# Kernel optimization log

Hardware: AMD Instinct MI355X
Metric: run time of the kernel (lower is better)

Reference implementation:

```python
import jax, jax.numpy as jnp
import numpy as np

BITS = 8
EPS = 1e-5
NUM_HEADS = 16


def ste_round(x):
    # straight-through rounding (matches brevitas round STE)
    return x + jax.lax.stop_gradient(jnp.round(x) - x)


def _scale(stat, qmax):
    return jnp.maximum(stat, 1e-8) / qmax


def fq_act_signed(x, bits=BITS):
    # runtime max-abs per-tensor scale (approximates brevitas runtime percentile 99.999)
    qmax = 2 ** (bits - 1) - 1
    qmin = -(2 ** (bits - 1))
    s = _scale(jnp.max(jnp.abs(x)), qmax)
    return jnp.clip(ste_round(x / s), qmin, qmax) * s


def fq_act_unsigned(x, bits=BITS):
    qmax = 2 ** bits - 1
    s = _scale(jnp.max(x), qmax)
    return jnp.clip(ste_round(x / s), 0, qmax) * s


def fq_weight(w, bits=BITS):
    # NarrowIntQuant + MaxStatsScaling: symmetric narrow range [-qmax, qmax]
    qmax = 2 ** (bits - 1) - 1
    s = _scale(jnp.max(jnp.abs(w)), qmax)
    return jnp.clip(ste_round(w / s), -qmax, qmax) * s


def fq_bias(b, bits=BITS):
    qmax = 2 ** (bits - 1) - 1
    qmin = -(2 ** (bits - 1))
    s = _scale(jnp.max(jnp.abs(b)), qmax)
    return jnp.clip(ste_round(b / s), qmin, qmax) * s


def layernorm(x):
    # elementwise_affine=False
    m = jnp.mean(x, axis=-1, keepdims=True)
    v = jnp.mean((x - m) ** 2, axis=-1, keepdims=True)
    return (x - m) / jnp.sqrt(v + EPS)


def setup_inputs() -> dict:
    key = jax.random.key(0)
    ks = jax.random.split(key, 13)
    B, S, E, M = 4, 1024, 1024, 4096
    std = 0.02
    inp = {
        "x": jax.random.normal(ks[0], (B, S, E), jnp.float32),
        "Wq": jax.random.normal(ks[1], (E, E), jnp.float32) * std,
        "bq": jax.random.normal(ks[2], (E,), jnp.float32) * std,
        "Wk": jax.random.normal(ks[3], (E, E), jnp.float32) * std,
        "bk": jax.random.normal(ks[4], (E,), jnp.float32) * std,
        "Wv": jax.random.normal(ks[5], (E, E), jnp.float32) * std,
        "bv": jax.random.normal(ks[6], (E,), jnp.float32) * std,
        "Wo": jax.random.normal(ks[7], (E, E), jnp.float32) * std,
        "bo": jax.random.normal(ks[8], (E,), jnp.float32) * std,
        "W1": jax.random.normal(ks[9], (M, E), jnp.float32) * std,
        "b1": jax.random.normal(ks[10], (M,), jnp.float32) * std,
        "W2": jax.random.normal(ks[11], (E, M), jnp.float32) * std,
        "b2": jax.random.normal(ks[12], (E,), jnp.float32) * std,
    }
    return inp


def reference(x, Wq, bq, Wk, bk, Wv, bv, Wo, bo, W1, b1, W2, b2):
    B, S, E = x.shape
    H = NUM_HEADS
    D = E // H
    # causal additive mask [S, S]
    i = jnp.arange(S)
    mask = jnp.where(i[None, :] <= i[:, None], 0.0, -jnp.inf).astype(x.dtype)

    # sdp_input_quant (shared q=k=v input)
    q_in = fq_act_signed(x)

    # quantized in-proj (packed_in_proj=False -> separate q/k/v projections)
    Q = q_in @ fq_weight(Wq).T + fq_bias(bq)
    K = q_in @ fq_weight(Wk).T + fq_bias(bk)
    V = q_in @ fq_weight(Wv).T + fq_bias(bv)

    Qh = Q.reshape(B, S, H, D)
    Kh = K.reshape(B, S, H, D)
    Vh = V.reshape(B, S, H, D)

    qs = fq_act_signed(Qh / jnp.sqrt(jnp.asarray(D, x.dtype)))  # q_scaled_quant
    kq = fq_act_signed(Kh)  # k_transposed_quant (per-tensor -> transpose-invariant)
    vq = fq_act_signed(Vh)  # v_quant

    scores = jnp.einsum("bqhd,bkhd->bhqk", qs, kq) + mask  # [B,H,S,S]
    attn = fq_act_signed(jax.nn.softmax(scores, axis=-1))  # attn_output_weights_quant

    ctx = jnp.einsum("bhqk,bkhd->bqhd", attn, vq).reshape(B, S, E)
    ctx = fq_act_signed(ctx)  # out_proj_input_quant
    attn_out = ctx @ fq_weight(Wo).T + fq_bias(bo)

    # residual_sdp: QuantEltwiseAdd quantizes both inputs, then layer-norm
    x1 = layernorm(fq_act_signed(x) + fq_act_signed(attn_out))

    # MLP: QuantIdentity -> QuantLinear -> QuantReLU -> QuantLinear
    h = fq_act_signed(x1) @ fq_weight(W1).T + fq_bias(b1)
    h = fq_act_unsigned(jax.nn.relu(h))
    h = h @ fq_weight(W2).T + fq_bias(b2)

    out = layernorm(fq_act_signed(x1) + fq_act_signed(h))
    return out
```

## Files before the change

### kernel.cpp

```cpp
#include <hip/hip_runtime.h>
#include <stdint.h>
#include <stddef.h>


typedef unsigned short u16;
typedef __attribute__((ext_vector_type(4))) int   i32x4;
typedef __attribute__((ext_vector_type(4))) float f32x4;

#define DEV __device__ __forceinline__

DEV float bf2f(u16 u) { return __uint_as_float(((unsigned)u) << 16); }
DEV void atomicMaxF(float* p, float v) { atomicMax((unsigned*)p, __float_as_uint(v)); }
DEV float waveMax(float v) {
#pragma unroll
  for (int o = 32; o; o >>= 1) v = fmaxf(v, __shfl_xor(v, o, 64));
  return v;
}
DEV float waveSum(float v) {
#pragma unroll
  for (int o = 32; o; o >>= 1) v += __shfl_xor(v, o, 64);
  return v;
}
DEV int waveSumI(int v) {
#pragma unroll
  for (int o = 32; o; o >>= 1) v += __shfl_xor(v, o, 64);
  return v;
}
DEV void blockStatMax(float v, float* __restrict__ slot64, float* sred4, int flatBlk) {
  v = waveMax(v);
  const int tid = threadIdx.x;
  if ((tid & 63) == 0) sred4[tid >> 6] = v;
  __syncthreads();
  if (tid == 0) {
    float m = fmaxf(fmaxf(sred4[0], sred4[1]), fmaxf(sred4[2], sred4[3]));
    atomicMaxF(&slot64[flatBlk & 63], m);
  }
}
DEV float slotMax64(const float* __restrict__ s) {
  float m = 0.f;
#pragma unroll
  for (int i = 0; i < 64; ++i) m = fmaxf(m, s[i]);
  return m;
}
DEV f32x4 ld4(const void* p, int i4, int isf32) {
  if (isf32) return ((const f32x4*)p)[i4];
  ushort4 u = ((const ushort4*)p)[i4];
  return (f32x4){bf2f(u.x), bf2f(u.y), bf2f(u.z), bf2f(u.w)};
}
DEV void gll16(const void* g, void* l) {
  __builtin_amdgcn_global_load_lds((__attribute__((address_space(1))) void*)(g),
                                   (__attribute__((address_space(3))) void*)(l),
                                   16, 0, 0);
}
DEV unsigned ldsaddr(const void* p) {
  return (unsigned)(size_t)(__attribute__((address_space(3))) const void*)p;
}
DEV unsigned quadsel(unsigned a, unsigned b, unsigned c, unsigned d, int idx) {
  unsigned lo = (idx & 1) ? b : a;
  unsigned hi = (idx & 1) ? d : c;
  return (idx & 2) ? hi : lo;
}

__global__ void detect_f32(const u16* __restrict__ x, int* __restrict__ flag) {
  const int tid = threadIdx.x;
  int cnt = 0;
#pragma unroll
  for (int i = 0; i < 16; ++i) {
    u16 u = x[tid * 16 + i];
    if ((u & 0x7f80u) >= 0x4380u) ++cnt;
  }
  cnt = waveSumI(cnt);
  if (tid == 0) flag[0] = (cnt > 16) ? 1 : 0;
}

struct AJobs { const void* p[13]; int n4[13]; int bstart[14]; };

__global__ __launch_bounds__(256) void absmax_multi(AJobs J, float* __restrict__ M,
                                                    const int* __restrict__ flagp) {
  __shared__ float sred[4];
  const int isf32 = flagp[0];
  const int blk = blockIdx.x, tid = threadIdx.x;
  int j = 0;
  while (j < 12 && blk >= J.bstart[j + 1]) ++j;
  const int lb = blk - J.bstart[j];
  const int nb = J.bstart[j + 1] - J.bstart[j];
  float mx = 0.f;
  const void* p = J.p[j];
  for (int i = lb * 256 + tid; i < J.n4[j]; i += nb * 256) {
    f32x4 v = ld4(p, i, isf32);
    mx = fmaxf(mx, fmaxf(fmaxf(fabsf(v.x), fabsf(v.y)),
                         fmaxf(fabsf(v.z), fabsf(v.w))));
  }
  blockStatMax(mx, M + j * 64, sred, lb);
}

__global__ __launch_bounds__(256) void quant_in_signed(
    const void* __restrict__ in, int8_t* __restrict__ out,
    const float* __restrict__ mp, const int* __restrict__ flagp, int n4) {
  const int isf32 = flagp[0];
  const float s = fmaxf(slotMax64(mp), 1e-8f) / 127.0f;
  char4* op = (char4*)out;
  for (int i = blockIdx.x * 256 + threadIdx.x; i < n4; i += gridDim.x * 256) {
    f32x4 v = ld4(in, i, isf32);
    char4 q;
    q.x = (signed char)fminf(fmaxf(rintf(v.x / s), -128.f), 127.f);
    q.y = (signed char)fminf(fmaxf(rintf(v.y / s), -128.f), 127.f);
    q.z = (signed char)fminf(fmaxf(rintf(v.z / s), -128.f), 127.f);
    q.w = (signed char)fminf(fmaxf(rintf(v.w / s), -128.f), 127.f);
    op[i] = q;
  }
}

struct WJobs { const void* in[5]; int8_t* out[5]; int mslot[5]; int n4[5]; int bstart[6]; };

__global__ __launch_bounds__(256) void quant_w_multi(WJobs J, const float* __restrict__ M,
                                                     const int* __restrict__ flagp) {
  const int isf32 = flagp[0];
  const int blk = blockIdx.x, tid = threadIdx.x;
  int j = 0;
  while (j < 4 && blk >= J.bstart[j + 1]) ++j;
  const int lb = blk - J.bstart[j];
  const int nb = J.bstart[j + 1] - J.bstart[j];
  const float s = fmaxf(slotMax64(M + J.mslot[j] * 64), 1e-8f) / 127.0f;
  const void* p = J.in[j];
  char4* o = (char4*)J.out[j];
  for (int i = lb * 256 + tid; i < J.n4[j]; i += nb * 256) {
    f32x4 v = ld4(p, i, isf32);
    char4 q;
    q.x = (signed char)fminf(fmaxf(rintf(v.x / s), -127.f), 127.f);
    q.y = (signed char)fminf(fmaxf(rintf(v.y / s), -127.f), 127.f);
    q.z = (signed char)fminf(fmaxf(rintf(v.z / s), -127.f), 127.f);
    q.w = (signed char)fminf(fmaxf(rintf(v.w / s), -127.f), 127.f);
    o[i] = q;
  }
}

__global__ __launch_bounds__(256) void quant_w2_rs(
    const void* __restrict__ w2, int8_t* __restrict__ out,
    const float* __restrict__ mp, const int* __restrict__ flagp,
    int* __restrict__ rowsum) {
  const int isf32 = flagp[0];
  const int row = blockIdx.x, tid = threadIdx.x;
  const float s = fmaxf(slotMax64(mp), 1e-8f) / 127.0f;
  char4* op = (char4*)(out + (size_t)row * 4096);
  int sum = 0;
  for (int i = tid; i < 1024; i += 256) {
    f32x4 v = ld4(w2, row * 1024 + i, isf32);
    char4 q;
    q.x = (signed char)fminf(fmaxf(rintf(v.x / s), -127.f), 127.f);
    q.y = (signed char)fminf(fmaxf(rintf(v.y / s), -127.f), 127.f);
    q.z = (signed char)fminf(fmaxf(rintf(v.z / s), -127.f), 127.f);
    q.w = (signed char)fminf(fmaxf(rintf(v.w / s), -127.f), 127.f);
    op[i] = q;
    sum += (int)q.x + (int)q.y + (int)q.z + (int)q.w;
  }
  sum = waveSumI(sum);
  __shared__ int rs4[4];
  if ((tid & 63) == 0) rs4[tid >> 6] = sum;
  __syncthreads();
  if (tid == 0) rowsum[row] = rs4[0] + rs4[1] + rs4[2] + rs4[3];
}

struct BJobs { const void* in[6]; float* out[6]; int mslot[6]; int n4[6]; };

__global__ __launch_bounds__(256) void fq_bias_multi(BJobs J, const float* __restrict__ M,
                                                     const int* __restrict__ flagp) {
  const int isf32 = flagp[0];
  const int j = blockIdx.x;
  const float s = fmaxf(slotMax64(M + J.mslot[j] * 64), 1e-8f) / 127.0f;
  float* o = J.out[j];
  for (int i = threadIdx.x; i < J.n4[j]; i += 256) {
    f32x4 v = ld4(J.in[j], i, isf32);
    f32x4 r;
    r.x = fminf(fmaxf(rintf(v.x / s), -128.f), 127.f) * s;
    r.y = fminf(fmaxf(rintf(v.y / s), -128.f), 127.f) * s;
    r.z = fminf(fmaxf(rintf(v.z / s), -128.f), 127.f) * s;
    r.w = fminf(fmaxf(rintf(v.w / s), -128.f), 127.f) * s;
    *(f32x4*)(o + i * 4) = r;
  }
}

__global__ __launch_bounds__(256) void quant_f32_signed(
    const float* __restrict__ in, int8_t* __restrict__ out,
    const float* __restrict__ mp, float pre, int n4) {
  const float s = fmaxf(slotMax64(mp) * pre, 1e-8f) / 127.0f;
  const f32x4* ip = (const f32x4*)in;
  char4* op = (char4*)out;
  for (int i = blockIdx.x * 256 + threadIdx.x; i < n4; i += gridDim.x * 256) {
    f32x4 v = ip[i];
    char4 q;
    q.x = (signed char)fminf(fmaxf(rintf(v.x * pre / s), -128.f), 127.f);
    q.y = (signed char)fminf(fmaxf(rintf(v.y * pre / s), -128.f), 127.f);
    q.z = (signed char)fminf(fmaxf(rintf(v.z * pre / s), -128.f), 127.f);
    q.w = (signed char)fminf(fmaxf(rintf(v.w * pre / s), -128.f), 127.f);
    op[i] = q;
  }
}

__global__ __launch_bounds__(256) void quant_f32_u8(
    const float* __restrict__ in, int8_t* __restrict__ out,
    const float* __restrict__ mp, int n4) {
  const float s = fmaxf(slotMax64(mp), 1e-8f) / 255.0f;
  const f32x4* ip = (const f32x4*)in;
  char4* op = (char4*)out;
  for (int i = blockIdx.x * 256 + threadIdx.x; i < n4; i += gridDim.x * 256) {
    f32x4 v = ip[i];
    char4 q;
    q.x = (signed char)((int)fminf(fmaxf(rintf(v.x / s), 0.f), 255.f) - 128);
    q.y = (signed char)((int)fminf(fmaxf(rintf(v.y / s), 0.f), 255.f) - 128);
    q.z = (signed char)((int)fminf(fmaxf(rintf(v.z / s), 0.f), 255.f) - 128);
    q.w = (signed char)((int)fminf(fmaxf(rintf(v.w / s), 0.f), 255.f) - 128);
    op[i] = q;
  }
}

__global__ __launch_bounds__(256) void quant_v_t(
    const float* __restrict__ V, int8_t* __restrict__ Vt,
    const float* __restrict__ mp) {
  __shared__ float tile[64][65];
  const int bh = blockIdx.x, st = blockIdx.y;
  const int b = bh >> 4, h = bh & 15;
  const int tid = threadIdx.x;
  const float s = fmaxf(slotMax64(mp), 1e-8f) / 127.0f;
  const int r = tid >> 2, c = (tid & 3) * 16;
  const float* src = V + ((size_t)(b * 1024 + st * 64 + r)) * 1024 + h * 64 + c;
#pragma unroll
  for (int g = 0; g < 4; ++g) {
    f32x4 v = *(const f32x4*)(src + g * 4);
    tile[r][c + g * 4 + 0] = v.x;
    tile[r][c + g * 4 + 1] = v.y;
    tile[r][c + g * 4 + 2] = v.z;
    tile[r][c + g * 4 + 3] = v.w;
  }
  __syncthreads();
  unsigned wds[4];
#pragma unroll
  for (int g = 0; g < 4; ++g) {
    unsigned wd = 0;
#pragma unroll
    for (int k = 0; k < 4; ++k) {
      float v = tile[c + g * 4 + k][r];
      int q = (int)fminf(fmaxf(rintf(v / s), -128.f), 127.f);
      wd |= ((unsigned)(unsigned char)(signed char)q) << (8 * k);
    }
    wds[g] = wd;
  }
  i32x4 ov = {(int)wds[0], (int)wds[1], (int)wds[2], (int)wds[3]};
  *(i32x4*)(Vt + ((size_t)((b * 16 + h) * 64 + r)) * 1024 + st * 64 + c) = ov;
}

__global__ __launch_bounds__(256) void gemm_i8(
    const int8_t* __restrict__ A, const int8_t* __restrict__ B,
    float* __restrict__ Cf, int8_t* __restrict__ Cq,
    const float* __restrict__ mA, float preA, float qmaxA,
    const float* __restrict__ mB,
    const float* __restrict__ bias, const int* __restrict__ extra,
    int relu, int mode, float* __restrict__ mOut, int K, int O) {
  __shared__ __align__(16) int8_t smem[4][12288];
  __shared__ float sred[4];
  const int tid = threadIdx.x;
  const int nb = blockIdx.x, ob = blockIdx.y;
  const int w = tid >> 6, lane = tid & 63, l15 = lane & 15, quad = lane >> 4;
  i32x4 acc[2][4];
#pragma unroll
  for (int i = 0; i < 2; ++i)
#pragma unroll
    for (int j = 0; j < 4; ++j) acc[i][j] = (i32x4){0, 0, 0, 0};
  const int r0 = tid >> 2;
  const int c0 = (((tid & 3) ^ ((tid >> 2) & 3)) * 16);
  const int8_t* Ab = A + (size_t)(nb * 128) * K;
  const int8_t* Bb = B + (size_t)(ob * 64) * K;
  const int nk = K >> 6;
  const int slot = (quad ^ (l15 & 3)) * 16;
  const int aoffl = (w * 32 + l15) * 64 + slot;
  const int boffl = 8192 + l15 * 64 + slot;
  for (int t = 0; t < 3 && t < nk; ++t) {
    const size_t kt0 = (size_t)t << 6;
    int8_t* d = smem[t];
    gll16(Ab + (size_t)r0 * K + kt0 + c0, d + tid * 16);
    gll16(Ab + (size_t)(r0 + 64) * K + kt0 + c0, d + 4096 + tid * 16);
    gll16(Bb + (size_t)r0 * K + kt0 + c0, d + 8192 + tid * 16);
  }
  for (int i = 0; i < nk; ++i) {
    const int infl = nk - 1 - i;
    if (infl >= 2)      asm volatile("s_waitcnt vmcnt(6)" ::: "memory");
    else if (infl == 1) asm volatile("s_waitcnt vmcnt(3)" ::: "memory");
    else                asm volatile("s_waitcnt vmcnt(0)" ::: "memory");
    asm volatile("s_barrier" ::: "memory");
    if (i + 3 < nk) {
      const size_t kt0 = (size_t)(i + 3) << 6;
      int8_t* d = smem[(i + 3) & 3];
      gll16(Ab + (size_t)r0 * K + kt0 + c0, d + tid * 16);
      gll16(Ab + (size_t)(r0 + 64) * K + kt0 + c0, d + 4096 + tid * 16);
      gll16(Bb + (size_t)r0 * K + kt0 + c0, d + 8192 + tid * 16);
    }
    const unsigned a_addr = ldsaddr(smem[i & 3] + aoffl);
    const unsigned b_addr = ldsaddr(smem[i & 3] + boffl);
    i32x4 af[2], bf[4];
    asm volatile("ds_read_b128 %0, %1 offset:0"    : "=v"(af[0]) : "v"(a_addr));
    asm volatile("ds_read_b128 %0, %1 offset:1024" : "=v"(af[1]) : "v"(a_addr));
    asm volatile("ds_read_b128 %0, %1 offset:0"    : "=v"(bf[0]) : "v"(b_addr));
    asm volatile("ds_read_b128 %0, %1 offset:1024" : "=v"(bf[1]) : "v"(b_addr));
    asm volatile("ds_read_b128 %0, %1 offset:2048" : "=v"(bf[2]) : "v"(b_addr));
    asm volatile("ds_read_b128 %0, %1 offset:3072" : "=v"(bf[3]) : "v"(b_addr));
    asm volatile("s_waitcnt lgkmcnt(0)" ::: "memory");
    __builtin_amdgcn_sched_barrier(0);
#pragma unroll
    for (int mt = 0; mt < 2; ++mt)
#pragma unroll
      for (int nt = 0; nt < 4; ++nt)
        acc[mt][nt] = __builtin_amdgcn_mfma_i32_16x16x64_i8(af[mt], bf[nt], acc[mt][nt], 0, 0, 0);
  }
  const float sA = fmaxf(slotMax64(mA) * preA, 1e-8f) / qmaxA;
  const float sB = fmaxf(slotMax64(mB), 1e-8f) / 127.0f;
  const float sAB = sA * sB;
  const float sq = (mode == 2) ? (fmaxf(slotMax64(mOut), 1e-8f) / 255.0f) : 1.0f;
  float lmax = 0.f;
#pragma unroll
  for (int mt = 0; mt < 2; ++mt) {
    const int n = nb * 128 + w * 32 + mt * 16 + quad * 4;
#pragma unroll
    for (int nt = 0; nt < 4; ++nt) {
      const int o = ob * 64 + nt * 16 + l15;
      const int ext = extra ? 128 * extra[o] : 0;
      const float bv = bias[o];
#pragma unroll
      for (int r = 0; r < 4; ++r) {
        float v = sAB * (float)(acc[mt][nt][r] + ext) + bv;
        if (relu) v = fmaxf(v, 0.f);
        if (mode == 0) Cf[(size_t)(n + r) * O + o] = v;
        else if (mode == 2) {
          int q = (int)fminf(fmaxf(rintf(v / sq), 0.f), 255.f) - 128;
          Cq[(size_t)(n + r) * O + o] = (int8_t)q;
        }
        lmax = fmaxf(lmax, fabsf(v));
      }
    }
  }
  if (mode != 2)
    blockStatMax(lmax, mOut, sred, nb + ob * gridDim.x);
}

__global__ __launch_bounds__(256, 4) void attn_fused(
    const int8_t* __restrict__ Qq, const int8_t* __restrict__ Kq,
    const int8_t* __restrict__ Vt, float* __restrict__ ctx,
    const float* __restrict__ M, float* __restrict__ mOut) {
  __shared__ __align__(16) int8_t qtile[4096];
  __shared__ __align__(16) int8_t ktile[4][4096];
  __shared__ __align__(16) int8_t vtile[4][4096];
  __shared__ float sred[4];
  const int tid = threadIdx.x, bid = blockIdx.x;
  const int pidx = bid & 7, rh = (bid >> 3) & 1, h = (bid >> 4) & 15, b = bid >> 8;
  const int qthi = 15 - pidx, qtlo = pidx, ktmax = qthi;
  const int w = tid >> 6, lane = tid & 63, l15 = lane & 15, quad = lane >> 4;
  const int wqt = (w < 2) ? qthi : qtlo;
  const int wrow0 = rh * 32 + (w & 1) * 16;
  const float sqs = fmaxf(slotMax64(M + 13 * 64) * 0.125f, 1e-8f) / 127.0f;
  const float sk = fmaxf(slotMax64(M + 14 * 64), 1e-8f) / 127.0f;
  const float sv = fmaxf(slotMax64(M + 15 * 64), 1e-8f) / 127.0f;
  const float sqk = sqs * sk;
  const float s_attn = 1.0f / 127.0f;
  const int r0 = tid >> 2;
  const int c0 = (((tid & 3) ^ ((tid >> 2) & 3)) * 16);
  const int8_t* Kbase = Kq + (size_t)(b * 1024) * 1024 + h * 64 + c0;
  const int8_t* Vbase = Vt + (size_t)((b * 16 + h) * 64 + r0) * 1024 + c0;
  const unsigned fragoff = (unsigned)(l15 * 64 + (quad ^ (l15 & 3)) * 16);

  {
    const int qt_s = (r0 < 32) ? qthi : qtlo;
    const int qrow_g = qt_s * 64 + rh * 32 + (r0 & 31);
    gll16(Qq + ((size_t)(b * 1024 + qrow_g)) * 1024 + h * 64 + c0, qtile + tid * 16);
  }
#pragma unroll
  for (int t = 0; t < 3; ++t)
    gll16(Kbase + (size_t)(t * 64 + r0) * 1024, ktile[t] + tid * 16);
  asm volatile("s_waitcnt vmcnt(3)" ::: "memory");
  asm volatile("s_barrier" ::: "memory");
  i32x4 aq;
  {
    const unsigned qa = ldsaddr(qtile) +
        (unsigned)((w * 16 + l15) * 64 + (quad ^ (l15 & 3)) * 16);
    asm volatile("ds_read_b128 %0, %1 offset:0" : "=v"(aq) : "v"(qa));
    asm volatile("s_waitcnt lgkmcnt(0)" ::: "memory");
  }
  const int qrow = wqt * 64 + wrow0 + l15;

  float m_l = -1e30f, l_l = 0.f;
  for (int kt = 0; kt <= ktmax; ++kt) {
    if (kt + 2 <= ktmax)      asm volatile("s_waitcnt vmcnt(2)" ::: "memory");
    else if (kt + 1 <= ktmax) asm volatile("s_waitcnt vmcnt(1)" ::: "memory");
    else                      asm volatile("s_waitcnt vmcnt(0)" ::: "memory");
    asm volatile("s_barrier" ::: "memory");
    if (kt + 3 <= ktmax)
      gll16(Kbase + (size_t)((kt + 3) * 64 + r0) * 1024, ktile[(kt + 3) & 3] + tid * 16);
    if (kt <= wqt) {
      const unsigned ka = ldsaddr(ktile[kt & 3]) + fragoff;
      i32x4 bk[4];
      asm volatile("ds_read_b128 %0, %1 offset:0"    : "=v"(bk[0]) : "v"(ka));
      asm volatile("ds_read_b128 %0, %1 offset:1024" : "=v"(bk[1]) : "v"(ka));
      asm volatile("ds_read_b128 %0, %1 offset:2048" : "=v"(bk[2]) : "v"(ka));
      asm volatile("ds_read_b128 %0, %1 offset:3072" : "=v"(bk[3]) : "v"(ka));
      asm volatile("s_waitcnt lgkmcnt(0)" ::: "memory");
      __builtin_amdgcn_sched_barrier(0);
      const int kc0 = kt * 64 + quad * 4;
      float sc[4][4];
#pragma unroll
      for (int nt = 0; nt < 4; ++nt) {
        i32x4 z = {0, 0, 0, 0};
        i32x4 d = __builtin_amdgcn_mfma_i32_16x16x64_i8(bk[nt], aq, z, 0, 0, 0);
        if (kt == wqt) {
#pragma unroll
          for (int r = 0; r < 4; ++r)
            sc[nt][r] = (kc0 + nt * 16 + r <= qrow) ? sqk * (float)d[r] : -1e30f;
        } else {
#pragma unroll
          for (int r = 0; r < 4; ++r) sc[nt][r] = sqk * (float)d[r];
        }
      }
      float vm = sc[0][0];
#pragma unroll
      for (int nt = 0; nt < 4; ++nt)
#pragma unroll
        for (int r = 0; r < 4; ++r) vm = fmaxf(vm, sc[nt][r]);
      const float mn = fmaxf(m_l, vm);
      float sum = 0.f;
#pragma unroll
      for (int nt = 0; nt < 4; ++nt)
#pragma unroll
        for (int r = 0; r < 4; ++r) sum += __expf(sc[nt][r] - mn);
      l_l = l_l * __expf(m_l - mn) + sum;
      m_l = mn;
    }
  }
#pragma unroll
  for (int off = 16; off <= 32; off <<= 1) {
    float om = __shfl_xor(m_l, off, 64);
    float ol = __shfl_xor(l_l, off, 64);
    float mn = fmaxf(m_l, om);
    l_l = l_l * __expf(m_l - mn) + ol * __expf(om - mn);
    m_l = mn;
  }
  const float rl127 = 127.0f / l_l;

  __syncthreads();
#pragma unroll
  for (int t = 0; t < 3; ++t) {
    gll16(Kbase + (size_t)(t * 64 + r0) * 1024, ktile[t] + tid * 16);
    gll16(Vbase + t * 64, vtile[t] + tid * 16);
  }
  i32x4 cacc[4] = {{0, 0, 0, 0}, {0, 0, 0, 0}, {0, 0, 0, 0}, {0, 0, 0, 0}};
  for (int kt = 0; kt <= ktmax; ++kt) {
    if (kt + 2 <= ktmax)      asm volatile("s_waitcnt vmcnt(4)" ::: "memory");
    else if (kt + 1 <= ktmax) asm volatile("s_waitcnt vmcnt(2)" ::: "memory");
    else                      asm volatile("s_waitcnt vmcnt(0)" ::: "memory");
    asm volatile("s_barrier" ::: "memory");
    if (kt + 3 <= ktmax) {
      gll16(Kbase + (size_t)((kt + 3) * 64 + r0) * 1024, ktile[(kt + 3) & 3] + tid * 16);
      gll16(Vbase + (kt + 3) * 64, vtile[(kt + 3) & 3] + tid * 16);
    }
    if (kt <= wqt) {
      const unsigned ka = ldsaddr(ktile[kt & 3]) + fragoff;
      const unsigned va = ldsaddr(vtile[kt & 3]) + fragoff;
      i32x4 bk[4], bv[4];
      asm volatile("ds_read_b128 %0, %1 offset:0"    : "=v"(bk[0]) : "v"(ka));
      asm volatile("ds_read_b128 %0, %1 offset:1024" : "=v"(bk[1]) : "v"(ka));
      asm volatile("ds_read_b128 %0, %1 offset:2048" : "=v"(bk[2]) : "v"(ka));
      asm volatile("ds_read_b128 %0, %1 offset:3072" : "=v"(bk[3]) : "v"(ka));
      asm volatile("ds_read_b128 %0, %1 offset:0"    : "=v"(bv[0]) : "v"(va));
      asm volatile("ds_read_b128 %0, %1 offset:1024" : "=v"(bv[1]) : "v"(va));
      asm volatile("ds_read_b128 %0, %1 offset:2048" : "=v"(bv[2]) : "v"(va));
      asm volatile("ds_read_b128 %0, %1 offset:3072" : "=v"(bv[3]) : "v"(va));
      asm volatile("s_waitcnt lgkmcnt(0)" ::: "memory");
      __builtin_amdgcn_sched_barrier(0);
      const int kc0 = kt * 64 + quad * 4;
      unsigned Dw[4];
#pragma unroll
      for (int nt = 0; nt < 4; ++nt) {
        i32x4 z = {0, 0, 0, 0};
        i32x4 d = __builtin_amdgcn_mfma_i32_16x16x64_i8(bk[nt], aq, z, 0, 0, 0);
        unsigned wd = 0;
        if (kt == wqt) {
#pragma unroll
          for (int r = 0; r < 4; ++r) {
            float e = (kc0 + nt * 16 + r <= qrow)
                          ? __expf(sqk * (float)d[r] - m_l) * rl127 : 0.f;
            wd |= ((unsigned)(int)rintf(e)) << (8 * r);
          }
        } else {
#pragma unroll
          for (int r = 0; r < 4; ++r) {
            float e = __expf(sqk * (float)d[r] - m_l) * rl127;
            wd |= ((unsigned)(int)rintf(e)) << (8 * r);
          }
        }
        Dw[nt] = wd;
      }
      unsigned selfv = quadsel(Dw[0], Dw[1], Dw[2], Dw[3], quad);
      unsigned rv1 = (unsigned)__shfl_xor(
          (int)quadsel(Dw[0], Dw[1], Dw[2], Dw[3], quad ^ 1), 16, 64);
      unsigned rv2 = (unsigned)__shfl_xor(
          (int)quadsel(Dw[0], Dw[1], Dw[2], Dw[3], quad ^ 2), 32, 64);
      unsigned rv3 = (unsigned)__shfl_xor(
          (int)quadsel(Dw[0], Dw[1], Dw[2], Dw[3], quad ^ 3), 48, 64);
      i32x4 pf;
#pragma unroll
      for (int j = 0; j < 4; ++j) {
        const int t = j ^ quad;
        pf[j] = (int)((t == 0) ? selfv : (t == 1) ? rv1 : (t == 2) ? rv2 : rv3);
      }
#pragma unroll
      for (int nt = 0; nt < 4; ++nt)
        cacc[nt] = __builtin_amdgcn_mfma_i32_16x16x64_i8(pf, bv[nt], cacc[nt], 0, 0, 0);
    }
  }
  const float sc2 = s_attn * sv;
  float lmax = 0.f;
  const int orow0 = wqt * 64 + wrow0 + quad * 4;
#pragma unroll
  for (int nt = 0; nt < 4; ++nt) {
    const int d = nt * 16 + l15;
#pragma unroll
    for (int r = 0; r < 4; ++r) {
      float v = sc2 * (float)cacc[nt][r];
      ctx[((size_t)(b * 1024 + orow0 + r)) * 1024 + h * 64 + d] = v;
      lmax = fmaxf(lmax, fabsf(v));
    }
  }
  blockStatMax(lmax, mOut, sred, bid);
}

__global__ __launch_bounds__(256) void ln_res(
    const int8_t* __restrict__ xq, const float* __restrict__ mx,
    const float* __restrict__ ao, const float* __restrict__ ma,
    float* __restrict__ x1, float* __restrict__ mOut) {
  __shared__ float red[8];
  __shared__ float sred[4];
  const int row = blockIdx.x, tid = threadIdx.x;
  const float sx = fmaxf(slotMax64(mx), 1e-8f) / 127.0f;
  const float sa = fmaxf(slotMax64(ma), 1e-8f) / 127.0f;
  char4 xv = *(const char4*)(xq + (size_t)row * 1024 + tid * 4);
  f32x4 av = *(const f32x4*)(ao + (size_t)row * 1024 + tid * 4);
  float t[4];
  t[0] = (float)xv.x * sx + fminf(fmaxf(rintf(av.x / sa), -128.f), 127.f) * sa;
  t[1] = (float)xv.y * sx + fminf(fmaxf(rintf(av.y / sa), -128.f), 127.f) * sa;
  t[2] = (float)xv.z * sx + fminf(fmaxf(rintf(av.z / sa), -128.f), 127.f) * sa;
  t[3] = (float)xv.w * sx + fminf(fmaxf(rintf(av.w / sa), -128.f), 127.f) * sa;
  float s = waveSum(t[0] + t[1] + t[2] + t[3]);
  if ((tid & 63) == 0) red[tid >> 6] = s;
  __syncthreads();
  const float mean = (red[0] + red[1] + red[2] + red[3]) * (1.0f / 1024.0f);
  float vs = 0.f;
#pragma unroll
  for (int i = 0; i < 4; ++i) { float d = t[i] - mean; vs += d * d; }
  vs = waveSum(vs);
  if ((tid & 63) == 0) red[4 + (tid >> 6)] = vs;
  __syncthreads();
  const float var = (red[4] + red[5] + red[6] + red[7]) * (1.0f / 1024.0f);
  const float rs = sqrtf(var + 1e-5f);
  f32x4 o;
  o.x = (t[0] - mean) / rs;
  o.y = (t[1] - mean) / rs;
  o.z = (t[2] - mean) / rs;
  o.w = (t[3] - mean) / rs;
  *(f32x4*)(x1 + (size_t)row * 1024 + tid * 4) = o;
  float lmax = fmaxf(fmaxf(fabsf(o.x), fabsf(o.y)), fmaxf(fabsf(o.z), fabsf(o.w)));
  blockStatMax(lmax, mOut, sred, row);
}

__global__ __launch_bounds__(256) void ln_final(
    const int8_t* __restrict__ x1q, const float* __restrict__ mx1,
    const float* __restrict__ h2, const float* __restrict__ mh2,
    float* __restrict__ out) {
  __shared__ float red[8];
  const int row = blockIdx.x, tid = threadIdx.x;
  const float s1 = fmaxf(slotMax64(mx1), 1e-8f) / 127.0f;
  const float s2 = fmaxf(slotMax64(mh2), 1e-8f) / 127.0f;
  char4 xv = *(const char4*)(x1q + (size_t)row * 1024 + tid * 4);
  f32x4 hv = *(const f32x4*)(h2 + (size_t)row * 1024 + tid * 4);
  float t[4];
  t[0] = (float)xv.x * s1 + fminf(fmaxf(rintf(hv.x / s2), -128.f), 127.f) * s2;
  t[1] = (float)xv.y * s1 + fminf(fmaxf(rintf(hv.y / s2), -128.f), 127.f) * s2;
  t[2] = (float)xv.z * s1 + fminf(fmaxf(rintf(hv.z / s2), -128.f), 127.f) * s2;
  t[3] = (float)xv.w * s1 + fminf(fmaxf(rintf(hv.w / s2), -128.f), 127.f) * s2;
  float s = waveSum(t[0] + t[1] + t[2] + t[3]);
  if ((tid & 63) == 0) red[tid >> 6] = s;
  __syncthreads();
  const float mean = (red[0] + red[1] + red[2] + red[3]) * (1.0f / 1024.0f);
  float vs = 0.f;
#pragma unroll
  for (int i = 0; i < 4; ++i) { float d = t[i] - mean; vs += d * d; }
  vs = waveSum(vs);
  if ((tid & 63) == 0) red[4 + (tid >> 6)] = vs;
  __syncthreads();
  const float var = (red[4] + red[5] + red[6] + red[7]) * (1.0f / 1024.0f);
  const float rs = sqrtf(var + 1e-5f);
  f32x4 o;
  o.x = (t[0] - mean) / rs;
  o.y = (t[1] - mean) / rs;
  o.z = (t[2] - mean) / rs;
  o.w = (t[3] - mean) / rs;
  *(f32x4*)(out + (size_t)row * 1024 + tid * 4) = o;
}

static constexpr size_t MB = 1u << 20;
static constexpr size_t OFF_M     = 0;
static constexpr size_t OFF_FLAG  = 6400;
static constexpr size_t OFF_BIASQ = 8192;
static constexpr size_t OFF_BIASK = OFF_BIASQ + 4096;
static constexpr size_t OFF_BIASV = OFF_BIASK + 4096;
static constexpr size_t OFF_BIASO = OFF_BIASV + 4096;
static constexpr size_t OFF_BIAS1 = OFF_BIASO + 4096;
static constexpr size_t OFF_BIAS2 = OFF_BIAS1 + 16384;
static constexpr size_t OFF_RS    = OFF_BIAS2 + 4096;
static constexpr size_t OFF_XQ    = 65536;
static constexpr size_t OFF_WQQ   = OFF_XQ  + 4 * MB;
static constexpr size_t OFF_WKQ   = OFF_WQQ + 1 * MB;
static constexpr size_t OFF_WVQ   = OFF_WKQ + 1 * MB;
static constexpr size_t OFF_WOQ   = OFF_WVQ + 1 * MB;
static constexpr size_t OFF_W1Q   = OFF_WOQ + 1 * MB;
static constexpr size_t OFF_W2Q   = OFF_W1Q + 4 * MB;
static constexpr size_t OFF_X1Q   = OFF_W2Q + 4 * MB;
static constexpr size_t OFF_A1    = OFF_X1Q + 4 * MB;
static constexpr size_t OFF_A2    = OFF_A1 + 16 * MB;
static constexpr size_t OFF_HF    = OFF_A2 + 16 * MB;

extern "C" void kernel_launch(void* const* d_in, const int* in_sizes, int n_in,
                              void* d_out, int out_size, void* d_ws, size_t ws_size,
                              hipStream_t stream) {
  (void)n_in; (void)out_size;
  char* ws = (char*)d_ws;
  float* M = (float*)(ws + OFF_M);
  int* FLAG = (int*)(ws + OFF_FLAG);
  float* BIASQ = (float*)(ws + OFF_BIASQ);
  float* BIASK = (float*)(ws + OFF_BIASK);
  float* BIASV = (float*)(ws + OFF_BIASV);
  float* BIASO = (float*)(ws + OFF_BIASO);
  float* BIAS1 = (float*)(ws + OFF_BIAS1);
  float* BIAS2 = (float*)(ws + OFF_BIAS2);
  int* RS = (int*)(ws + OFF_RS);
  int8_t* XQ  = (int8_t*)(ws + OFF_XQ);
  int8_t* WQQ = (int8_t*)(ws + OFF_WQQ);
  int8_t* WKQ = (int8_t*)(ws + OFF_WKQ);
  int8_t* WVQ = (int8_t*)(ws + OFF_WVQ);
  int8_t* WOQ = (int8_t*)(ws + OFF_WOQ);
  int8_t* W1Q = (int8_t*)(ws + OFF_W1Q);
  int8_t* W2Q = (int8_t*)(ws + OFF_W2Q);
  int8_t* X1Q = (int8_t*)(ws + OFF_X1Q);
  int8_t* QQ   = (int8_t*)(ws + OFF_A1);
  int8_t* KQQ  = (int8_t*)(ws + OFF_A1 + 4 * MB);
  int8_t* VT   = (int8_t*)(ws + OFF_A1 + 8 * MB);
  int8_t* CTXQ = (int8_t*)(ws + OFF_A1 + 12 * MB);
  float*  X1F  = (float*)(ws + OFF_A1);
  int8_t* HQ   = (int8_t*)(ws + OFF_A1);
  float* FBUF = (float*)(ws + OFF_A2);
  const bool bigws = ws_size >= OFF_HF + 64 * MB;

  hipMemsetAsync(M, 0, 8192, stream);
  detect_f32<<<1, 64, 0, stream>>>((const u16*)d_in[0], FLAG);

  AJobs aj;
  const int ablk[13] = {512, 128, 1, 128, 1, 128, 1, 128, 1, 512, 2, 512, 1};
  int bs = 0;
  for (int i = 0; i < 13; ++i) {
    aj.p[i] = d_in[i];
    aj.n4[i] = in_sizes[i] / 4;
    aj.bstart[i] = bs;
    bs += ablk[i];
  }
  aj.bstart[13] = bs;
  absmax_multi<<<bs, 256, 0, stream>>>(aj, M, FLAG);

  quant_in_signed<<<1024, 256, 0, stream>>>(d_in[0], XQ, M + 0 * 64, FLAG, in_sizes[0] / 4);

  WJobs wj;
  const int widx[5] = {1, 3, 5, 7, 9};
  int8_t* wout[5] = {WQQ, WKQ, WVQ, WOQ, W1Q};
  const int wblk[5] = {128, 128, 128, 128, 512};
  int wb = 0;
  for (int j = 0; j < 5; ++j) {
    wj.in[j] = d_in[widx[j]];
    wj.out[j] = wout[j];
    wj.mslot[j] = widx[j];
    wj.n4[j] = in_sizes[widx[j]] / 4;
    wj.bstart[j] = wb;
    wb += wblk[j];
  }
  wj.bstart[5] = wb;
  quant_w_multi<<<wb, 256, 0, stream>>>(wj, M, FLAG);
  quant_w2_rs<<<1024, 256, 0, stream>>>(d_in[11], W2Q, M + 11 * 64, FLAG, RS);

  BJobs bj;
  const int bidx[6] = {2, 4, 6, 8, 10, 12};
  float* bout[6] = {BIASQ, BIASK, BIASV, BIASO, BIAS1, BIAS2};
  for (int j = 0; j < 6; ++j) {
    bj.in[j] = d_in[bidx[j]];
    bj.out[j] = bout[j];
    bj.mslot[j] = bidx[j];
    bj.n4[j] = in_sizes[bidx[j]] / 4;
  }
  fq_bias_multi<<<6, 256, 0, stream>>>(bj, M, FLAG);

  gemm_i8<<<dim3(32, 16), 256, 0, stream>>>(XQ, WQQ, FBUF, nullptr, M + 0 * 64, 1.f, 127.f, M + 1 * 64, BIASQ, nullptr, 0, 0, M + 13 * 64, 1024, 1024);
  quant_f32_signed<<<2048, 256, 0, stream>>>(FBUF, QQ, M + 13 * 64, 0.125f, 1024 * 1024);
  gemm_i8<<<dim3(32, 16), 256, 0, stream>>>(XQ, WKQ, FBUF, nullptr, M + 0 * 64, 1.f, 127.f, M + 3 * 64, BIASK, nullptr, 0, 0, M + 14 * 64, 1024, 1024);
  quant_f32_signed<<<2048, 256, 0, stream>>>(FBUF, KQQ, M + 14 * 64, 1.0f, 1024 * 1024);
  gemm_i8<<<dim3(32, 16), 256, 0, stream>>>(XQ, WVQ, FBUF, nullptr, M + 0 * 64, 1.f, 127.f, M + 5 * 64, BIASV, nullptr, 0, 0, M + 15 * 64, 1024, 1024);
  quant_v_t<<<dim3(64, 16), 256, 0, stream>>>(FBUF, VT, M + 15 * 64);

  attn_fused<<<1024, 256, 0, stream>>>(QQ, KQQ, VT, FBUF, M, M + 16 * 64);
  quant_f32_signed<<<2048, 256, 0, stream>>>(FBUF, CTXQ, M + 16 * 64, 1.0f, 1024 * 1024);

  gemm_i8<<<dim3(32, 16), 256, 0, stream>>>(CTXQ, WOQ, FBUF, nullptr, M + 16 * 64, 1.f, 127.f, M + 7 * 64, BIASO, nullptr, 0, 0, M + 17 * 64, 1024, 1024);

  ln_res<<<4096, 256, 0, stream>>>(XQ, M + 0 * 64, FBUF, M + 17 * 64, X1F, M + 18 * 64);
  quant_f32_signed<<<2048, 256, 0, stream>>>(X1F, X1Q, M + 18 * 64, 1.0f, 1024 * 1024);

  if (bigws) {
    float* HF = (float*)(ws + OFF_HF);
    gemm_i8<<<dim3(32, 64), 256, 0, stream>>>(X1Q, W1Q, HF, nullptr, M + 18 * 64, 1.f, 127.f, M + 9 * 64, BIAS1, nullptr, 1, 0, M + 19 * 64, 1024, 4096);
    quant_f32_u8<<<2048, 256, 0, stream>>>(HF, HQ, M + 19 * 64, 4096 * 1024);
  } else {
    gemm_i8<<<dim3(32, 64), 256, 0, stream>>>(X1Q, W1Q, nullptr, nullptr, M + 18 * 64, 1.f, 127.f, M + 9 * 64, BIAS1, nullptr, 1, 1, M + 19 * 64, 1024, 4096);
    gemm_i8<<<dim3(32, 64), 256, 0, stream>>>(X1Q, W1Q, nullptr, HQ,      M + 18 * 64, 1.f, 127.f, M + 9 * 64, BIAS1, nullptr, 1, 2, M + 19 * 64, 1024, 4096);
  }

  gemm_i8<<<dim3(32, 16), 256, 0, stream>>>(HQ, W2Q, FBUF, nullptr, M + 19 * 64, 1.f, 255.f, M + 11 * 64, BIAS2, RS, 0, 0, M + 20 * 64, 4096, 1024);

  ln_final<<<4096, 256, 0, stream>>>(X1Q, M + 18 * 64, FBUF, M + 20 * 64, (float*)d_out);
}
```

Before: 409.8 us.

## Fuse Q/K/V projection GEMMs into one launch and shrink GEMM LDS ring to three stages

On the large-workspace path, the three Q, K and V projection GEMMs become one launch with a 48-wide output grid. Each block selects its region (output buffer, weight scale slot, stat slot) from its column-block index, which relies on WQQ, WKQ, WVQ and their biases being laid out contiguously. Separately, the GEMM software pipeline drops from four LDS buffers with prefetch depth three to three buffers with depth two. The aim is to cut launches and fill the GPU better, and to lower LDS use for higher occupancy, at the cost of less latency hiding.

```diff
diff --git a/kernel.cpp b/kernel.cpp
--- a/kernel.cpp
+++ b/kernel.cpp
@@ -255,8 +255,8 @@
     const float* __restrict__ mA, float preA, float qmaxA,
     const float* __restrict__ mB,
     const float* __restrict__ bias, const int* __restrict__ extra,
-    int relu, int mode, float* __restrict__ mOut, int K, int O) {
-  __shared__ __align__(16) int8_t smem[4][12288];
+    int relu, int mode, int qkv, float* __restrict__ mOut, int K, int O) {
+  __shared__ __align__(16) int8_t smem[3][12288];
   __shared__ float sred[4];
   const int tid = threadIdx.x;
   const int nb = blockIdx.x, ob = blockIdx.y;
@@ -274,28 +274,29 @@
   const int slot = (quad ^ (l15 & 3)) * 16;
   const int aoffl = (w * 32 + l15) * 64 + slot;
   const int boffl = 8192 + l15 * 64 + slot;
-  for (int t = 0; t < 3 && t < nk; ++t) {
+  for (int t = 0; t < 2 && t < nk; ++t) {
     const size_t kt0 = (size_t)t << 6;
     int8_t* d = smem[t];
     gll16(Ab + (size_t)r0 * K + kt0 + c0, d + tid * 16);
     gll16(Ab + (size_t)(r0 + 64) * K + kt0 + c0, d + 4096 + tid * 16);
     gll16(Bb + (size_t)r0 * K + kt0 + c0, d + 8192 + tid * 16);
   }
+  int cb = 0, ib = 2;
   for (int i = 0; i < nk; ++i) {
-    const int infl = nk - 1 - i;
-    if (infl >= 2)      asm volatile("s_waitcnt vmcnt(6)" ::: "memory");
-    else if (infl == 1) asm volatile("s_waitcnt vmcnt(3)" ::: "memory");
-    else                asm volatile("s_waitcnt vmcnt(0)" ::: "memory");
+    if (i + 1 < nk) asm volatile("s_waitcnt vmcnt(3)" ::: "memory");
+    else            asm volatile("s_waitcnt vmcnt(0)" ::: "memory");
     asm volatile("s_barrier" ::: "memory");
-    if (i + 3 < nk) {
-      const size_t kt0 = (size_t)(i + 3) << 6;
-      int8_t* d = smem[(i + 3) & 3];
+    if (i + 2 < nk) {
+      const size_t kt0 = (size_t)(i + 2) << 6;
+      int8_t* d = smem[ib];
       gll16(Ab + (size_t)r0 * K + kt0 + c0, d + tid * 16);
       gll16(Ab + (size_t)(r0 + 64) * K + kt0 + c0, d + 4096 + tid * 16);
       gll16(Bb + (size_t)r0 * K + kt0 + c0, d + 8192 + tid * 16);
+      ib = (ib == 2) ? 0 : ib + 1;
     }
-    const unsigned a_addr = ldsaddr(smem[i & 3] + aoffl);
-    const unsigned b_addr = ldsaddr(smem[i & 3] + boffl);
+    const unsigned a_addr = ldsaddr(smem[cb] + aoffl);
+    const unsigned b_addr = ldsaddr(smem[cb] + boffl);
+    cb = (cb == 2) ? 0 : cb + 1;
     i32x4 af[2], bf[4];
     asm volatile("ds_read_b128 %0, %1 offset:0"    : "=v"(af[0]) : "v"(a_addr));
     asm volatile("ds_read_b128 %0, %1 offset:1024" : "=v"(af[1]) : "v"(a_addr));
@@ -311,6 +312,12 @@
       for (int nt = 0; nt < 4; ++nt)
         acc[mt][nt] = __builtin_amdgcn_mfma_i32_16x16x64_i8(af[mt], bf[nt], acc[mt][nt], 0, 0, 0);
   }
+  const int region = qkv ? (ob >> 4) : 0;
+  if (qkv) {
+    Cf += (size_t)region << 22;
+    mB += region * 128;
+    mOut += region * 64;
+  }
   const float sA = fmaxf(slotMax64(mA) * preA, 1e-8f) / qmaxA;
   const float sB = fmaxf(slotMax64(mB), 1e-8f) / 127.0f;
   const float sAB = sA * sB;
@@ -322,23 +329,24 @@
 #pragma unroll
     for (int nt = 0; nt < 4; ++nt) {
       const int o = ob * 64 + nt * 16 + l15;
+      const int oc = qkv ? (o & 1023) : o;
       const int ext = extra ? 128 * extra[o] : 0;
       const float bv = bias[o];
 #pragma unroll
       for (int r = 0; r < 4; ++r) {
         float v = sAB * (float)(acc[mt][nt][r] + ext) + bv;
         if (relu) v = fmaxf(v, 0.f);
-        if (mode == 0) Cf[(size_t)(n + r) * O + o] = v;
+        if (mode == 0) Cf[(size_t)(n + r) * O + oc] = v;
         else if (mode == 2) {
           int q = (int)fminf(fmaxf(rintf(v / sq), 0.f), 255.f) - 128;
-          Cq[(size_t)(n + r) * O + o] = (int8_t)q;
+          Cq[(size_t)(n + r) * O + oc] = (int8_t)q;
         }
         lmax = fmaxf(lmax, fabsf(v));
       }
     }
   }
   if (mode != 2)
-    blockStatMax(lmax, mOut, sred, nb + ob * gridDim.x);
+    blockStatMax(lmax, mOut, sred, nb + (qkv ? (ob & 15) : ob) * gridDim.x);
 }
 
 __global__ __launch_bounds__(256, 4) void attn_fused(
@@ -700,31 +708,39 @@
   }
   fq_bias_multi<<<6, 256, 0, stream>>>(bj, M, FLAG);
 
-  gemm_i8<<<dim3(32, 16), 256, 0, stream>>>(XQ, WQQ, FBUF, nullptr, M + 0 * 64, 1.f, 127.f, M + 1 * 64, BIASQ, nullptr, 0, 0, M + 13 * 64, 1024, 1024);
-  quant_f32_signed<<<2048, 256, 0, stream>>>(FBUF, QQ, M + 13 * 64, 0.125f, 1024 * 1024);
-  gemm_i8<<<dim3(32, 16), 256, 0, stream>>>(XQ, WKQ, FBUF, nullptr, M + 0 * 64, 1.f, 127.f, M + 3 * 64, BIASK, nullptr, 0, 0, M + 14 * 64, 1024, 1024);
-  quant_f32_signed<<<2048, 256, 0, stream>>>(FBUF, KQQ, M + 14 * 64, 1.0f, 1024 * 1024);
-  gemm_i8<<<dim3(32, 16), 256, 0, stream>>>(XQ, WVQ, FBUF, nullptr, M + 0 * 64, 1.f, 127.f, M + 5 * 64, BIASV, nullptr, 0, 0, M + 15 * 64, 1024, 1024);
-  quant_v_t<<<dim3(64, 16), 256, 0, stream>>>(FBUF, VT, M + 15 * 64);
+  if (bigws) {
+    float* HF = (float*)(ws + OFF_HF);
+    gemm_i8<<<dim3(32, 48), 256, 0, stream>>>(XQ, WQQ, HF, nullptr, M + 0 * 64, 1.f, 127.f, M + 1 * 64, BIASQ, nullptr, 0, 0, 1, M + 13 * 64, 1024, 1024);
+    quant_f32_signed<<<2048, 256, 0, stream>>>(HF, QQ, M + 13 * 64, 0.125f, 1024 * 1024);
+    quant_f32_signed<<<2048, 256, 0, stream>>>(HF + (1u << 22), KQQ, M + 14 * 64, 1.0f, 1024 * 1024);
+    quant_v_t<<<dim3(64, 16), 256, 0, stream>>>(HF + (2u << 22), VT, M + 15 * 64);
+  } else {
+    gemm_i8<<<dim3(32, 16), 256, 0, stream>>>(XQ, WQQ, FBUF, nullptr, M + 0 * 64, 1.f, 127.f, M + 1 * 64, BIASQ, nullptr, 0, 0, 0, M + 13 * 64, 1024, 1024);
+    quant_f32_signed<<<2048, 256, 0, stream>>>(FBUF, QQ, M + 13 * 64, 0.125f, 1024 * 1024);
+    gemm_i8<<<dim3(32, 16), 256, 0, stream>>>(XQ, WKQ, FBUF, nullptr, M + 0 * 64, 1.f, 127.f, M + 3 * 64, BIASK, nullptr, 0, 0, 0, M + 14 * 64, 1024, 1024);
+    quant_f32_signed<<<2048, 256, 0, stream>>>(FBUF, KQQ, M + 14 * 64, 1.0f, 1024 * 1024);
+    gemm_i8<<<dim3(32, 16), 256, 0, stream>>>(XQ, WVQ, FBUF, nullptr, M + 0 * 64, 1.f, 127.f, M + 5 * 64, BIASV, nullptr, 0, 0, 0, M + 15 * 64, 1024, 1024);
+    quant_v_t<<<dim3(64, 16), 256, 0, stream>>>(FBUF, VT, M + 15 * 64);
+  }
 
   attn_fused<<<1024, 256, 0, stream>>>(QQ, KQQ, VT, FBUF, M, M + 16 * 64);
   quant_f32_signed<<<2048, 256, 0, stream>>>(FBUF, CTXQ, M + 16 * 64, 1.0f, 1024 * 1024);
 
-  gemm_i8<<<dim3(32, 16), 256, 0, stream>>>(CTXQ, WOQ, FBUF, nullptr, M + 16 * 64, 1.f, 127.f, M + 7 * 64, BIASO, nullptr, 0, 0, M + 17 * 64, 1024, 1024);
+  gemm_i8<<<dim3(32, 16), 256, 0, stream>>>(CTXQ, WOQ, FBUF, nullptr, M + 16 * 64, 1.f, 127.f, M + 7 * 64, BIASO, nullptr, 0, 0, 0, M + 17 * 64, 1024, 1024);
 
   ln_res<<<4096, 256, 0, stream>>>(XQ, M + 0 * 64, FBUF, M + 17 * 64, X1F, M + 18 * 64);
   quant_f32_signed<<<2048, 256, 0, stream>>>(X1F, X1Q, M + 18 * 64, 1.0f, 1024 * 1024);
 
   if (bigws) {
     float* HF = (float*)(ws + OFF_HF);
-    gemm_i8<<<dim3(32, 64), 256, 0, stream>>>(X1Q, W1Q, HF, nullptr, M + 18 * 64, 1.f, 127.f, M + 9 * 64, BIAS1, nullptr, 1, 0, M + 19 * 64, 1024, 4096);
+    gemm_i8<<<dim3(32, 64), 256, 0, stream>>>(X1Q, W1Q, HF, nullptr, M + 18 * 64, 1.f, 127.f, M + 9 * 64, BIAS1, nullptr, 1, 0, 0, M + 19 * 64, 1024, 4096);
     quant_f32_u8<<<2048, 256, 0, stream>>>(HF, HQ, M + 19 * 64, 4096 * 1024);
   } else {
-    gemm_i8<<<dim3(32, 64), 256, 0, stream>>>(X1Q, W1Q, nullptr, nullptr, M + 18 * 64, 1.f, 127.f, M + 9 * 64, BIAS1, nullptr, 1, 1, M + 19 * 64, 1024, 4096);
-    gemm_i8<<<dim3(32, 64), 256, 0, stream>>>(X1Q, W1Q, nullptr, HQ,      M + 18 * 64, 1.f, 127.f, M + 9 * 64, BIAS1, nullptr, 1, 2, M + 19 * 64, 1024, 4096);
-  }
-
-  gemm_i8<<<dim3(32, 16), 256, 0, stream>>>(HQ, W2Q, FBUF, nullptr, M + 19 * 64, 1.f, 255.f, M + 11 * 64, BIAS2, RS, 0, 0, M + 20 * 64, 4096, 1024);
+    gemm_i8<<<dim3(32, 64), 256, 0, stream>>>(X1Q, W1Q, nullptr, nullptr, M + 18 * 64, 1.f, 127.f, M + 9 * 64, BIAS1, nullptr, 1, 1, 0, M + 19 * 64, 1024, 4096);
+    gemm_i8<<<dim3(32, 64), 256, 0, stream>>>(X1Q, W1Q, nullptr, HQ,      M + 18 * 64, 1.f, 127.f, M + 9 * 64, BIAS1, nullptr, 1, 2, 0, M + 19 * 64, 1024, 4096);
+  }
+
+  gemm_i8<<<dim3(32, 16), 256, 0, stream>>>(HQ, W2Q, FBUF, nullptr, M + 19 * 64, 1.f, 255.f, M + 11 * 64, BIAS2, RS, 0, 0, 0, M + 20 * 64, 4096, 1024);
 
   ln_final<<<4096, 256, 0, stream>>>(X1Q, M + 18 * 64, FBUF, M + 20 * 64, (float*)d_out);
 }
```

After: 386.6 us. 1.06x faster.
